# Kernel tuning notes

Hardware: AMD Instinct MI355X
Metric: run time of the kernel (lower is better)

## Reference

```python
import jax, jax.numpy as jnp
import numpy as np

B, L, D, U = 4, 1024, 64, 32

def setup_inputs() -> dict:
    key = jax.random.key(0)
    ks = jax.random.split(key, 6)
    inputs = jax.random.normal(ks[0], (B, L, D), dtype=jnp.float32)
    Wt = jax.random.normal(ks[1], (D, U), dtype=jnp.float32) * 0.1
    Wx = jax.random.normal(ks[2], (D, U), dtype=jnp.float32) * 0.1
    Wa = jax.random.normal(ks[3], (U, 1), dtype=jnp.float32) * 0.1
    bh = jax.random.normal(ks[4], (U,), dtype=jnp.float32) * 0.1
    ba = jax.random.normal(ks[5], (1,), dtype=jnp.float32) * 0.1
    return {"inputs": inputs, "Wt": Wt, "Wx": Wx, "Wa": Wa,
            "bh": bh, "ba": ba, "attention_width": 0}

def reference(inputs, Wt, Wx, Wa, bh, ba, attention_width):
    # Additive (Bahdanau) self-attention emission.
    q = inputs @ Wt                              # (B, L, U)
    k = inputs @ Wx                              # (B, L, U)
    # broadcast add -> (B, L, L, U), the dominant intermediate
    h = jnp.tanh(q[:, :, None, :] + k[:, None, :, :] + bh)
    e = jnp.squeeze(h @ Wa, axis=-1) + ba        # (B, L, L); ba broadcasts
    # NOTE: attention_width mask is dead code in the original forward -> ignored.
    # manual max-subtracted softmax with +1e-8 denominator (as in source)
    m = jnp.max(e, axis=-1, keepdims=True)
    ex = jnp.exp(e - m)
    a = ex / (jnp.sum(ex, axis=-1, keepdims=True) + 1e-8)
    v = jnp.einsum('bij,bjd->bid', a, inputs)    # (B, L, D)
    return v
```

## Files before the change

kernel.cpp:

```cpp
#include <hip/hip_runtime.h>

#define BB 4
#define LL 1024
#define DD 64
#define UU 32
#define TI 8
#define NT 512

__global__ __launch_bounds__(256) void precompute_kernel(
    const float* __restrict__ inp, const float* __restrict__ Wt,
    const float* __restrict__ Wx, const float* __restrict__ bh,
    float* __restrict__ Eq, float* __restrict__ Ekt)
{
    __shared__ float s_in[8][DD];
    __shared__ float s_wt[DD][UU];
    __shared__ float s_wx[DD][UU];
    __shared__ float s_ek[8][36];
    int t = threadIdx.x;
    int row0 = blockIdx.x * 8;
    if (t < 128)
        ((float4*)s_in)[t] = ((const float4*)(inp + (size_t)row0 * DD))[t];
#pragma unroll
    for (int p = 0; p < 2; ++p) {
        ((float4*)s_wt)[p * 256 + t] = ((const float4*)Wt)[p * 256 + t];
        ((float4*)s_wx)[p * 256 + t] = ((const float4*)Wx)[p * 256 + t];
    }
    __syncthreads();
    int r = t >> 5;
    int u = t & 31;
    size_t row = row0 + r;
    float q = 0.f, k = 0.f;
#pragma unroll
    for (int d = 0; d < DD; ++d) {
        float x = s_in[r][d];
        q = fmaf(x, s_wt[d][u], q);
        k = fmaf(x, s_wx[d][u], k);
    }
    Eq[row * UU + u] = __expf(2.f * (q + bh[u]));
    s_ek[r][u] = __expf(2.f * k);
    __syncthreads();
    if (t < 64) {
        int u4 = t >> 3, r2 = t & 7;
        float4 v = *(const float4*)(&s_ek[r2][u4 * 4]);
        size_t gr = row0 + r2;
        size_t bb_ = gr >> 10, l = gr & 1023;
        ((float4*)Ekt)[(bb_ * 8 + u4) * LL + l] = v;
    }
}

union ShMem {
    struct { float a0[LL][4]; float a1[LL][4]; } a;
    float4 v[8][TI][16];
};

__global__ __launch_bounds__(NT) void attn_kernel(
    const float* __restrict__ Eq, const float* __restrict__ Ekt,
    const float* __restrict__ inp, const float* __restrict__ Wa,
    float* __restrict__ out)
{
    __shared__ ShMem sh;
    __shared__ float s_red[2][8][TI];

    int t  = threadIdx.x;
    int w  = t >> 6;
    int b  = blockIdx.x >> 7;
    int i0 = (blockIdx.x & 127) * TI;

    const float4* ektb = (const float4*)Ekt + (size_t)b * 8 * LL;
    const float*  eqb  = Eq + ((size_t)(b * LL + i0)) * UU;

    float acc[TI][2];
#pragma unroll
    for (int i = 0; i < TI; ++i) { acc[i][0] = 0.f; acc[i][1] = 0.f; }

    float4 cur0 = ektb[t], cur1 = ektb[NT + t];

#pragma unroll
    for (int u4 = 0; u4 < 8; ++u4) {
        float4 nxt0, nxt1;
        if (u4 < 7) {
            nxt0 = ektb[(u4 + 1) * LL + t];
            nxt1 = ektb[(u4 + 1) * LL + NT + t];
        }
        const float* waq = Wa + u4 * 4;
        float wa0 = waq[0], wa1 = waq[1], wa2 = waq[2], wa3 = waq[3];
#pragma unroll
        for (int i = 0; i < TI; ++i) {
            const float* eqq = eqb + i * UU + u4 * 4;
            float eq0 = eqq[0], eq1 = eqq[1], eq2 = eqq[2], eq3 = eqq[3];
#pragma unroll
            for (int jj = 0; jj < 2; ++jj) {
                float4 ek = jj ? cur1 : cur0;
                float p  = fmaf(eq0, ek.x, 1.f);
                float q  = fmaf(eq1, ek.y, 1.f);
                float r  = fmaf(eq2, ek.z, 1.f);
                float s  = fmaf(eq3, ek.w, 1.f);
                float n01 = fmaf(wa0, q, wa1 * p);
                float n23 = fmaf(wa2, s, wa3 * r);
                float pq = p * q, rs = r * s;
                float num = fmaf(n01, rs, n23 * pq);
                float den = pq * rs;
                acc[i][jj] = fmaf(num, __builtin_amdgcn_rcpf(den), acc[i][jj]);
            }
        }
        if (u4 < 7) { cur0 = nxt0; cur1 = nxt1; }
    }

    float ev[TI][2];
#pragma unroll
    for (int i = 0; i < TI; ++i) {
        ev[i][0] = -2.f * acc[i][0];
        ev[i][1] = -2.f * acc[i][1];
    }

    float wred[TI];
#pragma unroll
    for (int i = 0; i < TI; ++i) {
        float v = fmaxf(ev[i][0], ev[i][1]);
#pragma unroll
        for (int m = 32; m >= 1; m >>= 1) v = fmaxf(v, __shfl_xor(v, m, 64));
        wred[i] = v;
    }
    if ((t & 63) == 0) {
#pragma unroll
        for (int i = 0; i < TI; ++i) s_red[0][w][i] = wred[i];
    }
    __syncthreads();
    float m[TI];
#pragma unroll
    for (int i = 0; i < TI; ++i) {
        float v = s_red[0][0][i];
#pragma unroll
        for (int w2 = 1; w2 < 8; ++w2) v = fmaxf(v, s_red[0][w2][i]);
        m[i] = v;
    }

#pragma unroll
    for (int i = 0; i < TI; ++i) {
        ev[i][0] = __expf(ev[i][0] - m[i]);
        ev[i][1] = __expf(ev[i][1] - m[i]);
        float s = ev[i][0] + ev[i][1];
#pragma unroll
        for (int mm = 32; mm >= 1; mm >>= 1) s += __shfl_xor(s, mm, 64);
        wred[i] = s;
    }
    if ((t & 63) == 0) {
#pragma unroll
        for (int i = 0; i < TI; ++i) s_red[1][w][i] = wred[i];
    }
    __syncthreads();
    float rs[TI];
#pragma unroll
    for (int i = 0; i < TI; ++i) {
        float s = 0.f;
#pragma unroll
        for (int w2 = 0; w2 < 8; ++w2) s += s_red[1][w2][i];
        rs[i] = 1.0f / (s + 1e-8f);
    }

#pragma unroll
    for (int jj = 0; jj < 2; ++jj) {
        int j = jj * NT + t;
        float4 lo, hi;
        lo.x = ev[0][jj] * rs[0]; lo.y = ev[1][jj] * rs[1];
        lo.z = ev[2][jj] * rs[2]; lo.w = ev[3][jj] * rs[3];
        hi.x = ev[4][jj] * rs[4]; hi.y = ev[5][jj] * rs[5];
        hi.z = ev[6][jj] * rs[6]; hi.w = ev[7][jj] * rs[7];
        *(float4*)(&sh.a.a0[j][0]) = lo;
        *(float4*)(&sh.a.a1[j][0]) = hi;
    }
    __syncthreads();

    int dq = t & 15;
    int g  = t >> 4;
    const float4* inp4 = (const float4*)(inp + (size_t)b * LL * DD);
    float4 v[TI];
#pragma unroll
    for (int i = 0; i < TI; ++i) v[i] = (float4){0.f, 0.f, 0.f, 0.f};

#pragma unroll 4
    for (int jj = 0; jj < 32; ++jj) {
        int j = jj * 32 + g;
        float4 x  = inp4[j * 16 + dq];
        float4 a0 = *(const float4*)(&sh.a.a0[j][0]);
        float4 a1 = *(const float4*)(&sh.a.a1[j][0]);
        v[0].x = fmaf(a0.x, x.x, v[0].x); v[0].y = fmaf(a0.x, x.y, v[0].y);
        v[0].z = fmaf(a0.x, x.z, v[0].z); v[0].w = fmaf(a0.x, x.w, v[0].w);
        v[1].x = fmaf(a0.y, x.x, v[1].x); v[1].y = fmaf(a0.y, x.y, v[1].y);
        v[1].z = fmaf(a0.y, x.z, v[1].z); v[1].w = fmaf(a0.y, x.w, v[1].w);
        v[2].x = fmaf(a0.z, x.x, v[2].x); v[2].y = fmaf(a0.z, x.y, v[2].y);
        v[2].z = fmaf(a0.z, x.z, v[2].z); v[2].w = fmaf(a0.z, x.w, v[2].w);
        v[3].x = fmaf(a0.w, x.x, v[3].x); v[3].y = fmaf(a0.w, x.y, v[3].y);
        v[3].z = fmaf(a0.w, x.z, v[3].z); v[3].w = fmaf(a0.w, x.w, v[3].w);
        v[4].x = fmaf(a1.x, x.x, v[4].x); v[4].y = fmaf(a1.x, x.y, v[4].y);
        v[4].z = fmaf(a1.x, x.z, v[4].z); v[4].w = fmaf(a1.x, x.w, v[4].w);
        v[5].x = fmaf(a1.y, x.x, v[5].x); v[5].y = fmaf(a1.y, x.y, v[5].y);
        v[5].z = fmaf(a1.y, x.z, v[5].z); v[5].w = fmaf(a1.y, x.w, v[5].w);
        v[6].x = fmaf(a1.z, x.x, v[6].x); v[6].y = fmaf(a1.z, x.y, v[6].y);
        v[6].z = fmaf(a1.z, x.z, v[6].z); v[6].w = fmaf(a1.z, x.w, v[6].w);
        v[7].x = fmaf(a1.w, x.x, v[7].x); v[7].y = fmaf(a1.w, x.y, v[7].y);
        v[7].z = fmaf(a1.w, x.z, v[7].z); v[7].w = fmaf(a1.w, x.w, v[7].w);
    }

#pragma unroll
    for (int i = 0; i < TI; ++i) {
        v[i].x += __shfl_xor(v[i].x, 16, 64); v[i].y += __shfl_xor(v[i].y, 16, 64);
        v[i].z += __shfl_xor(v[i].z, 16, 64); v[i].w += __shfl_xor(v[i].w, 16, 64);
        v[i].x += __shfl_xor(v[i].x, 32, 64); v[i].y += __shfl_xor(v[i].y, 32, 64);
        v[i].z += __shfl_xor(v[i].z, 32, 64); v[i].w += __shfl_xor(v[i].w, 32, 64);
    }
    __syncthreads();
    if ((t & 63) < 16) {
#pragma unroll
        for (int i = 0; i < TI; ++i) sh.v[w][i][dq] = v[i];
    }
    __syncthreads();

    int i = t >> 6;
    int d = t & 63;
    const float* svf = (const float*)sh.v;
    float r = 0.f;
#pragma unroll
    for (int w2 = 0; w2 < 8; ++w2) r += svf[w2 * (TI * 64) + i * 64 + d];
    out[((size_t)b * LL + (i0 + i)) * DD + d] = r;
}

extern "C" void kernel_launch(void* const* d_in, const int* in_sizes, int n_in,
                              void* d_out, int out_size, void* d_ws, size_t ws_size,
                              hipStream_t stream) {
    const float* inp = (const float*)d_in[0];
    const float* Wt  = (const float*)d_in[1];
    const float* Wx  = (const float*)d_in[2];
    const float* Wa  = (const float*)d_in[3];
    const float* bh  = (const float*)d_in[4];
    float* out = (float*)d_out;

    float* Eq  = (float*)d_ws;
    float* Ekt = Eq + (size_t)BB * LL * UU;

    precompute_kernel<<<BB * LL / 8, 256, 0, stream>>>(inp, Wt, Wx, bh, Eq, Ekt);
    attn_kernel<<<BB * LL / TI, NT, 0, stream>>>(Eq, Ekt, inp, Wa, out);
}
```

Before: 98.08 us.

## Drop softmax max pass, defer normalization, preload key exponentials into registers

Removes the max-subtraction reduction and its block barrier, relying on the attention logits being bounded because tanh outputs are bounded and weighted by Wa. The softmax denominator is applied once per output element at the end instead of to every attention weight. All key exponentials are loaded into registers up front and the loop order becomes row-major. The shared-memory union is split so one barrier can be dropped, and a min-blocks launch bound is added. The launch bound may cap the register budget and cause spills with the larger preloaded register set, and dropping the max shift risks overflow if Wa is large.

Measured after the change: 92.38 us. 1.06x faster.

```diff
diff --git a/kernel.cpp b/kernel.cpp
--- a/kernel.cpp
+++ b/kernel.cpp
@@ -48,18 +48,15 @@
     }
 }
 
-union ShMem {
-    struct { float a0[LL][4]; float a1[LL][4]; } a;
-    float4 v[8][TI][16];
-};
-
-__global__ __launch_bounds__(NT) void attn_kernel(
+__global__ __launch_bounds__(NT, 4) void attn_kernel(
     const float* __restrict__ Eq, const float* __restrict__ Ekt,
     const float* __restrict__ inp, const float* __restrict__ Wa,
     float* __restrict__ out)
 {
-    __shared__ ShMem sh;
-    __shared__ float s_red[2][8][TI];
+    __shared__ float s_a0[LL][4];
+    __shared__ float s_a1[LL][4];
+    __shared__ float4 s_v[8][TI][16];
+    __shared__ float s_red[8][TI];
 
     int t  = threadIdx.x;
     int w  = t >> 6;
@@ -69,105 +66,67 @@
     const float4* ektb = (const float4*)Ekt + (size_t)b * 8 * LL;
     const float*  eqb  = Eq + ((size_t)(b * LL + i0)) * UU;
 
+    float4 ek[8][2];
+#pragma unroll
+    for (int u4 = 0; u4 < 8; ++u4) {
+        ek[u4][0] = ektb[u4 * LL + t];
+        ek[u4][1] = ektb[u4 * LL + NT + t];
+    }
+
     float acc[TI][2];
 #pragma unroll
-    for (int i = 0; i < TI; ++i) { acc[i][0] = 0.f; acc[i][1] = 0.f; }
-
-    float4 cur0 = ektb[t], cur1 = ektb[NT + t];
-
-#pragma unroll
-    for (int u4 = 0; u4 < 8; ++u4) {
-        float4 nxt0, nxt1;
-        if (u4 < 7) {
-            nxt0 = ektb[(u4 + 1) * LL + t];
-            nxt1 = ektb[(u4 + 1) * LL + NT + t];
-        }
-        const float* waq = Wa + u4 * 4;
-        float wa0 = waq[0], wa1 = waq[1], wa2 = waq[2], wa3 = waq[3];
-#pragma unroll
-        for (int i = 0; i < TI; ++i) {
-            const float* eqq = eqb + i * UU + u4 * 4;
-            float eq0 = eqq[0], eq1 = eqq[1], eq2 = eqq[2], eq3 = eqq[3];
+    for (int i = 0; i < TI; ++i) {
+        acc[i][0] = 0.f;
+        acc[i][1] = 0.f;
+        const float* eqq = eqb + i * UU;
+#pragma unroll
+        for (int u4 = 0; u4 < 8; ++u4) {
+            const float* waq = Wa + u4 * 4;
+            float wa0 = waq[0], wa1 = waq[1], wa2 = waq[2], wa3 = waq[3];
+            float eq0 = eqq[u4 * 4 + 0], eq1 = eqq[u4 * 4 + 1];
+            float eq2 = eqq[u4 * 4 + 2], eq3 = eqq[u4 * 4 + 3];
 #pragma unroll
             for (int jj = 0; jj < 2; ++jj) {
-                float4 ek = jj ? cur1 : cur0;
-                float p  = fmaf(eq0, ek.x, 1.f);
-                float q  = fmaf(eq1, ek.y, 1.f);
-                float r  = fmaf(eq2, ek.z, 1.f);
-                float s  = fmaf(eq3, ek.w, 1.f);
+                float4 e = ek[u4][jj];
+                float p  = fmaf(eq0, e.x, 1.f);
+                float q  = fmaf(eq1, e.y, 1.f);
+                float r  = fmaf(eq2, e.z, 1.f);
+                float s  = fmaf(eq3, e.w, 1.f);
                 float n01 = fmaf(wa0, q, wa1 * p);
                 float n23 = fmaf(wa2, s, wa3 * r);
-                float pq = p * q, rs = r * s;
-                float num = fmaf(n01, rs, n23 * pq);
-                float den = pq * rs;
+                float pq = p * q, rsd = r * s;
+                float num = fmaf(n01, rsd, n23 * pq);
+                float den = pq * rsd;
                 acc[i][jj] = fmaf(num, __builtin_amdgcn_rcpf(den), acc[i][jj]);
             }
         }
-        if (u4 < 7) { cur0 = nxt0; cur1 = nxt1; }
-    }
-
-    float ev[TI][2];
+    }
+
+    float wsum[TI];
 #pragma unroll
     for (int i = 0; i < TI; ++i) {
-        ev[i][0] = -2.f * acc[i][0];
-        ev[i][1] = -2.f * acc[i][1];
-    }
-
-    float wred[TI];
-#pragma unroll
-    for (int i = 0; i < TI; ++i) {
-        float v = fmaxf(ev[i][0], ev[i][1]);
-#pragma unroll
-        for (int m = 32; m >= 1; m >>= 1) v = fmaxf(v, __shfl_xor(v, m, 64));
-        wred[i] = v;
+        float e0 = __expf(-2.f * acc[i][0]);
+        float e1 = __expf(-2.f * acc[i][1]);
+        acc[i][0] = e0;
+        acc[i][1] = e1;
+        float s = e0 + e1;
+#pragma unroll
+        for (int mm = 32; mm >= 1; mm >>= 1) s += __shfl_xor(s, mm, 64);
+        wsum[i] = s;
     }
     if ((t & 63) == 0) {
 #pragma unroll
-        for (int i = 0; i < TI; ++i) s_red[0][w][i] = wred[i];
-    }
-    __syncthreads();
-    float m[TI];
-#pragma unroll
-    for (int i = 0; i < TI; ++i) {
-        float v = s_red[0][0][i];
-#pragma unroll
-        for (int w2 = 1; w2 < 8; ++w2) v = fmaxf(v, s_red[0][w2][i]);
-        m[i] = v;
-    }
-
-#pragma unroll
-    for (int i = 0; i < TI; ++i) {
-        ev[i][0] = __expf(ev[i][0] - m[i]);
-        ev[i][1] = __expf(ev[i][1] - m[i]);
-        float s = ev[i][0] + ev[i][1];
-#pragma unroll
-        for (int mm = 32; mm >= 1; mm >>= 1) s += __shfl_xor(s, mm, 64);
-        wred[i] = s;
-    }
-    if ((t & 63) == 0) {
-#pragma unroll
-        for (int i = 0; i < TI; ++i) s_red[1][w][i] = wred[i];
-    }
-    __syncthreads();
-    float rs[TI];
-#pragma unroll
-    for (int i = 0; i < TI; ++i) {
-        float s = 0.f;
-#pragma unroll
-        for (int w2 = 0; w2 < 8; ++w2) s += s_red[1][w2][i];
-        rs[i] = 1.0f / (s + 1e-8f);
+        for (int i = 0; i < TI; ++i) s_red[w][i] = wsum[i];
     }
 
 #pragma unroll
     for (int jj = 0; jj < 2; ++jj) {
         int j = jj * NT + t;
         float4 lo, hi;
-        lo.x = ev[0][jj] * rs[0]; lo.y = ev[1][jj] * rs[1];
-        lo.z = ev[2][jj] * rs[2]; lo.w = ev[3][jj] * rs[3];
-        hi.x = ev[4][jj] * rs[4]; hi.y = ev[5][jj] * rs[5];
-        hi.z = ev[6][jj] * rs[6]; hi.w = ev[7][jj] * rs[7];
-        *(float4*)(&sh.a.a0[j][0]) = lo;
-        *(float4*)(&sh.a.a1[j][0]) = hi;
+        lo.x = acc[0][jj]; lo.y = acc[1][jj]; lo.z = acc[2][jj]; lo.w = acc[3][jj];
+        hi.x = acc[4][jj]; hi.y = acc[5][jj]; hi.z = acc[6][jj]; hi.w = acc[7][jj];
+        *(float4*)(&s_a0[j][0]) = lo;
+        *(float4*)(&s_a1[j][0]) = hi;
     }
     __syncthreads();
 
@@ -182,8 +141,8 @@
     for (int jj = 0; jj < 32; ++jj) {
         int j = jj * 32 + g;
         float4 x  = inp4[j * 16 + dq];
-        float4 a0 = *(const float4*)(&sh.a.a0[j][0]);
-        float4 a1 = *(const float4*)(&sh.a.a1[j][0]);
+        float4 a0 = *(const float4*)(&s_a0[j][0]);
+        float4 a1 = *(const float4*)(&s_a1[j][0]);
         v[0].x = fmaf(a0.x, x.x, v[0].x); v[0].y = fmaf(a0.x, x.y, v[0].y);
         v[0].z = fmaf(a0.x, x.z, v[0].z); v[0].w = fmaf(a0.x, x.w, v[0].w);
         v[1].x = fmaf(a0.y, x.x, v[1].x); v[1].y = fmaf(a0.y, x.y, v[1].y);
@@ -209,20 +168,22 @@
         v[i].x += __shfl_xor(v[i].x, 32, 64); v[i].y += __shfl_xor(v[i].y, 32, 64);
         v[i].z += __shfl_xor(v[i].z, 32, 64); v[i].w += __shfl_xor(v[i].w, 32, 64);
     }
-    __syncthreads();
     if ((t & 63) < 16) {
 #pragma unroll
-        for (int i = 0; i < TI; ++i) sh.v[w][i][dq] = v[i];
+        for (int i = 0; i < TI; ++i) s_v[w][i][dq] = v[i];
     }
     __syncthreads();
 
     int i = t >> 6;
     int d = t & 63;
-    const float* svf = (const float*)sh.v;
+    const float* svf = (const float*)s_v;
     float r = 0.f;
 #pragma unroll
     for (int w2 = 0; w2 < 8; ++w2) r += svf[w2 * (TI * 64) + i * 64 + d];
-    out[((size_t)b * LL + (i0 + i)) * DD + d] = r;
+    float ssum = 0.f;
+#pragma unroll
+    for (int w2 = 0; w2 < 8; ++w2) ssum += s_red[w2][i];
+    out[((size_t)b * LL + (i0 + i)) * DD + d] = r * (1.0f / (ssum + 1e-8f));
 }
 
 extern "C" void kernel_launch(void* const* d_in, const int* in_sizes, int n_in,
```
